# Kernel optimization log

Hardware: AMD Instinct MI355X
Metric: run time of the kernel (lower is better)

The kernel has to match this reference:

```python
import jax, jax.numpy as jnp
import numpy as np

B, L, D, H = 2, 2048, 512, 8
HS = D // H          # head_size = 64
BLOCK = 2048         # block_size
EPS = 1e-5


def setup_inputs() -> dict:
    key = jax.random.key(0)
    ks = jax.random.split(key, 8)
    s = 0.02
    x = jax.random.normal(ks[0], (B, L, D), jnp.float32)
    mask = jnp.triu(jnp.ones((1, 1, L, L), bool), k=1)  # causal: True above diag
    wq = jax.random.normal(ks[1], (D, D), jnp.float32) * s
    wk = jax.random.normal(ks[2], (D, D), jnp.float32) * s
    wv = jax.random.normal(ks[3], (D, D), jnp.float32) * s
    wo = jax.random.normal(ks[4], (D, D), jnp.float32) * s
    Er = jax.random.normal(ks[5], (H, BLOCK, HS), jnp.float32)
    bq = jnp.zeros((D,), jnp.float32)
    bk = jnp.zeros((D,), jnp.float32)
    bv = jnp.zeros((D,), jnp.float32)
    bo = jnp.zeros((D,), jnp.float32)
    ln_g = jnp.ones((D,), jnp.float32)
    ln_b = jnp.zeros((D,), jnp.float32)
    return dict(x=x, mask=mask, ln_g=ln_g, ln_b=ln_b, wq=wq, bq=bq,
                wk=wk, bk=bk, wv=wv, bv=bv, wo=wo, bo=bo, Er=Er)


def _skew(qe):
    # qe: [B, H, L, L] -> pad last dim on the left, reshape trick, drop first row
    padded = jnp.pad(qe, ((0, 0), (0, 0), (0, 0), (1, 0)))
    b, h, l, l1 = padded.shape
    return padded.reshape(b, h, l1, l)[:, :, 1:, :]


def reference(x, mask, ln_g, ln_b, wq, bq, wk, bk, wv, bv, wo, bo, Er):
    l = x.shape[1]
    # LayerNorm
    mu = jnp.mean(x, axis=-1, keepdims=True)
    var = jnp.mean((x - mu) ** 2, axis=-1, keepdims=True)
    hn = (x - mu) / jnp.sqrt(var + EPS) * ln_g + ln_b
    # QKV: [B, H, L, HS]
    q = (hn @ wq.T + bq).reshape(-1, l, H, HS).transpose(0, 2, 1, 3)
    k = (hn @ wk.T + bk).reshape(-1, l, H, HS).transpose(0, 2, 1, 3)
    v = (hn @ wv.T + bv).reshape(-1, l, H, HS).transpose(0, 2, 1, 3)
    # relative position bias via skew
    Ers = Er[:, BLOCK - l:, :]                       # [H, l, HS]
    QEr = jnp.einsum('bhld,hmd->bhlm', q, Ers)       # [B, H, L, L]
    SRel = _skew(QEr)
    # scaled dot-product scores
    w = jnp.einsum('bhld,bhmd->bhlm', q, k) * (HS ** -0.5)
    w = jnp.where(mask, -jnp.inf, w)
    SRel = jnp.where(mask, -jnp.inf, SRel)
    w = jax.nn.softmax(w + SRel, axis=-1)            # dropout omitted (eval mode)
    out = jnp.einsum('bhlm,bhmd->bhld', w, v)
    out = out.transpose(0, 2, 1, 3).reshape(-1, l, D)
    return out @ wo.T + bo
```

## Files before the change

kernel.cpp:

```cpp
#include <hip/hip_runtime.h>

#define LSEQ 2048
#define DIM 512
#define NH 8
#define HS 64

typedef __attribute__((ext_vector_type(8))) short short8;
typedef __attribute__((ext_vector_type(4))) float f32x4;

__device__ inline unsigned short f2bf(float f) {
  union { float f; unsigned u; } a; a.f = f;
  unsigned r = a.u + 0x7FFFu + ((a.u >> 16) & 1u);
  return (unsigned short)(r >> 16);
}
__device__ inline float bf2f(unsigned short h) {
  union { unsigned u; float f; } a; a.u = ((unsigned)h) << 16;
  return a.f;
}
__device__ inline unsigned cvtpk(float lo, float hi) {
  unsigned r;
  asm("v_cvt_pk_bf16_f32 %0, %1, %2" : "=v"(r) : "v"(lo), "v"(hi));
  return r;
}

__device__ inline f32x4 mfma_bf16(short8 a, short8 b, f32x4 c) {
  return __builtin_amdgcn_mfma_f32_16x16x32_bf16(a, b, c, 0, 0, 0);
}

__device__ inline short8 ld8(const unsigned short* p) {
  return *reinterpret_cast<const short8*>(p);
}

#define GLLDS(SRC, DST) __builtin_amdgcn_global_load_lds( \
    (const __attribute__((address_space(1))) void*)(SRC), \
    (__attribute__((address_space(3))) void*)(DST), 16, 0, 0)

__global__ __launch_bounds__(256) void cvt_all_kernel(
    const float* __restrict__ wq, const float* __restrict__ wk,
    const float* __restrict__ wv, const float* __restrict__ wo,
    const float* __restrict__ Er,
    unsigned short* __restrict__ wqb, unsigned short* __restrict__ wkb,
    unsigned short* __restrict__ wvb, unsigned short* __restrict__ wob,
    unsigned short* __restrict__ erb) {
  int b = blockIdx.x;
  const float* src; unsigned short* dst; int off;
  float scl = 1.f;
  if (b < 256)       { src = wq; dst = wqb; off = b; }
  else if (b < 512)  { src = wk; dst = wkb; off = b - 256; }
  else if (b < 768)  { src = wv; dst = wvb; off = b - 512; }
  else if (b < 1024) { src = wo; dst = wob; off = b - 768; }
  else               { src = Er; dst = erb; off = b - 1024; scl = 1.4426950408889634f; }
  int i = (off * 256 + threadIdx.x) * 4;
  float4 v = *reinterpret_cast<const float4*>(src + i);
  unsigned lo = (unsigned)f2bf(v.x * scl) | ((unsigned)f2bf(v.y * scl) << 16);
  unsigned hi = (unsigned)f2bf(v.z * scl) | ((unsigned)f2bf(v.w * scl) << 16);
  uint2 pk; pk.x = lo; pk.y = hi;
  *reinterpret_cast<uint2*>(dst + i) = pk;
}

__global__ __launch_bounds__(256) void ln_kernel(const float* __restrict__ x,
    const float* __restrict__ g, const float* __restrict__ bta,
    unsigned short* __restrict__ hn) {
  int lane = threadIdx.x & 63, w = threadIdx.x >> 6;
  int row = blockIdx.x * 4 + w;
  const float4* xr = reinterpret_cast<const float4*>(x + (size_t)row * DIM);
  float4 a = xr[2 * lane], c = xr[2 * lane + 1];
  float s = a.x + a.y + a.z + a.w + c.x + c.y + c.z + c.w;
  float sq = a.x * a.x + a.y * a.y + a.z * a.z + a.w * a.w +
             c.x * c.x + c.y * c.y + c.z * c.z + c.w * c.w;
#pragma unroll
  for (int off = 1; off < 64; off <<= 1) {
    s += __shfl_xor(s, off);
    sq += __shfl_xor(sq, off);
  }
  float mu = s * (1.f / DIM);
  float var = sq * (1.f / DIM) - mu * mu;
  float rstd = rsqrtf(var + 1e-5f);
  float4 g0 = reinterpret_cast<const float4*>(g)[2 * lane];
  float4 g1 = reinterpret_cast<const float4*>(g)[2 * lane + 1];
  float4 b0 = reinterpret_cast<const float4*>(bta)[2 * lane];
  float4 b1 = reinterpret_cast<const float4*>(bta)[2 * lane + 1];
  uint4 o;
  o.x = (unsigned)f2bf((a.x - mu) * rstd * g0.x + b0.x) |
        ((unsigned)f2bf((a.y - mu) * rstd * g0.y + b0.y) << 16);
  o.y = (unsigned)f2bf((a.z - mu) * rstd * g0.z + b0.z) |
        ((unsigned)f2bf((a.w - mu) * rstd * g0.w + b0.w) << 16);
  o.z = (unsigned)f2bf((c.x - mu) * rstd * g1.x + b1.x) |
        ((unsigned)f2bf((c.y - mu) * rstd * g1.y + b1.y) << 16);
  o.w = (unsigned)f2bf((c.z - mu) * rstd * g1.z + b1.z) |
        ((unsigned)f2bf((c.w - mu) * rstd * g1.w + b1.w) << 16);
  reinterpret_cast<uint4*>(hn)[(size_t)row * 64 + lane] = o;
}

__global__ __launch_bounds__(256, 3) void qkv_kernel(const unsigned short* __restrict__ hn,
    const unsigned short* __restrict__ wqb, const unsigned short* __restrict__ wkb,
    const unsigned short* __restrict__ wvb,
    const float* __restrict__ bq, const float* __restrict__ bk, const float* __restrict__ bv,
    unsigned short* __restrict__ qo, unsigned short* __restrict__ ko,
    unsigned short* __restrict__ vT) {
  __shared__ unsigned short As[3][128 * 32];
  __shared__ unsigned short Bs[3][128 * 32];
  int tid = threadIdx.x, lane = tid & 63, w = tid >> 6;
  int mcol = lane & 15, grp = lane >> 4;
  int l4 = lane >> 2, lql = lane & 3;
  int bid = blockIdx.x;
  int mat = bid >> 7;
  int rem = bid & 127;
  int m0 = (rem >> 2) << 7;
  int n0 = (rem & 3) << 7;
  const unsigned short* W = (mat == 0) ? wqb : (mat == 1) ? wkb : wvb;
  const float* bias = (mat == 0) ? bq : (mat == 1) ? bk : bv;
  float scl = (mat == 1) ? 0.18033688011112042f : 1.f;
  int wr = w >> 1, wc = w & 1;

  f32x4 acc[4][4];
#pragma unroll
  for (int i = 0; i < 4; ++i)
#pragma unroll
    for (int j = 0; j < 4; ++j) acc[i][j] = (f32x4){0.f, 0.f, 0.f, 0.f};

#pragma unroll
  for (int j = 0; j < 2; ++j) {
    int row = 32 * w + 16 * j + l4;
    GLLDS(hn + (size_t)(m0 + row) * DIM + lql * 8, &As[0][(32 * w + 16 * j) * 32]);
    GLLDS(W + (size_t)(n0 + row) * DIM + lql * 8, &Bs[0][(32 * w + 16 * j) * 32]);
  }
  for (int kk = 0; kk < 16; ++kk) {
    int buf = kk % 3;
    if (kk < 15) {
      int nbuf = (kk + 1) % 3;
      int k0 = (kk + 1) * 32;
#pragma unroll
      for (int j = 0; j < 2; ++j) {
        int row = 32 * w + 16 * j + l4;
        GLLDS(hn + (size_t)(m0 + row) * DIM + k0 + lql * 8, &As[nbuf][(32 * w + 16 * j) * 32]);
        GLLDS(W + (size_t)(n0 + row) * DIM + k0 + lql * 8, &Bs[nbuf][(32 * w + 16 * j) * 32]);
      }
      asm volatile("s_waitcnt vmcnt(4)\n\ts_barrier" ::: "memory");
    } else {
      asm volatile("s_waitcnt vmcnt(0)\n\ts_barrier" ::: "memory");
    }
    const unsigned short* AL = As[buf];
    const unsigned short* BL = Bs[buf];
    short8 af[4], bf[4];
#pragma unroll
    for (int f = 0; f < 4; ++f) {
      af[f] = ld8(&AL[(wr * 64 + f * 16 + mcol) * 32 + grp * 8]);
      bf[f] = ld8(&BL[(wc * 64 + f * 16 + mcol) * 32 + grp * 8]);
    }
#pragma unroll
    for (int fi = 0; fi < 4; ++fi)
#pragma unroll
      for (int fj = 0; fj < 4; ++fj)
        acc[fi][fj] = mfma_bf16(af[fi], bf[fj], acc[fi][fj]);
  }
#pragma unroll
  for (int fj = 0; fj < 4; ++fj) {
    int n = n0 + wc * 64 + fj * 16 + mcol;
    int hh = n >> 6, d = n & 63;
    float bsv = bias[n];
#pragma unroll
    for (int fi = 0; fi < 4; ++fi) {
#pragma unroll
      for (int r = 0; r < 4; ++r) {
        int m = m0 + wr * 64 + fi * 16 + 4 * grp + r;
        float val = (acc[fi][fj][r] + bsv) * scl;
        int b = m >> 11, l = m & (LSEQ - 1);
        unsigned short hv = f2bf(val);
        if (mat == 2) {
          size_t base = (size_t)(b * NH + hh) * HS * LSEQ;
          int idx = (((l >> 5) * 4 + (d >> 4)) * 64 + ((l >> 3) & 3) * 16 + (d & 15)) * 8 + (l & 7);
          vT[base + idx] = hv;
        } else {
          unsigned short* dst = (mat == 0) ? qo : ko;
          dst[((size_t)(b * NH + hh) * LSEQ + l) * HS + d] = hv;
        }
      }
    }
  }
}

__global__ __launch_bounds__(256, 2) void attn_kernel(const unsigned short* __restrict__ q,
    const unsigned short* __restrict__ k, const unsigned short* __restrict__ vT,
    const unsigned short* __restrict__ erb, char* __restrict__ partials) {
  __shared__ unsigned short Kt[2][64 * 64];
  __shared__ unsigned short Ers[320 * 64];
  __shared__ float Uall[4][16 * 84];
  int tid = threadIdx.x, lane = tid & 63, w = tid >> 6;
  int mcol = lane & 15, grp = lane >> 4;
  float* U = Uall[w];

  int bid = blockIdx.x;
  int xcd = bid & 7, s = bid >> 3;
  int hi2 = (s >= 80) ? 1 : 0;
  int bh = xcd + 8 * hi2;
  int ub = 79 - (s - 80 * hi2);
  int gp = (ub < 8) ? 0 : (ub < 24) ? 1 : (ub < 48) ? 2 : 3;
  int st0 = (gp == 0) ? 0 : (gp == 1) ? 8 : (gp == 2) ? 24 : 48;
  int idx = ub - st0;
  int tq = idx / (gp + 1);
  int cc = idx - tq * (gp + 1);
  int t64 = 8 * gp + tq;
  int qi0 = t64 << 6;
  int c0 = cc << 9;
  int kend = min(c0 + 512, qi0 + 64);
  int nkb = (kend - c0 + 63) >> 6;
  int h = bh & 7;

  const unsigned short* Qb = q + (size_t)bh * LSEQ * HS;
  const unsigned short* Kb = k + (size_t)bh * LSEQ * HS;
  const unsigned short* Vb = vT + (size_t)bh * HS * LSEQ;
  const unsigned short* Eb = erb + (size_t)h * LSEQ * HS;

  int qi0w = qi0 + 16 * w;
  short8 qf0 = ld8(Qb + (size_t)(qi0w + mcol) * HS + 8 * grp);
  short8 qf1 = ld8(Qb + (size_t)(qi0w + mcol) * HS + 32 + 8 * grp);
  int Estart = 2032 - qi0 - 48 + c0;
  int l8 = lane >> 3, lg = lane & 7;

#pragma unroll
  for (int j = 0; j < 2; ++j) {
    int row = 16 * w + 8 * j + l8;
    const unsigned short* src = Kb + (size_t)(c0 + row) * HS + (lg ^ (row & 7)) * 8;
    GLLDS(src, &Kt[0][(16 * w + 8 * j) * 64]);
  }
#pragma unroll
  for (int j = 0; j < 6; ++j) {
    int relb = 48 * w + 8 * j;
    int er = Estart + relb + l8;
    int erc = min(er, 2047);
    const unsigned short* src = Eb + (size_t)erc * HS + (lg ^ (er & 7)) * 8;
    GLLDS(src, &Ers[relb * 64]);
  }

  f32x4 o[4];
#pragma unroll
  for (int i = 0; i < 4; ++i) o[i] = (f32x4){0.f, 0.f, 0.f, 0.f};
  float lacc = 0.f;
  int srcA = mcol | ((grp & 1) << 5);
  int srcB = srcA + 16;
  bool hi = (grp >= 2);
  int efsw = mcol & 7;
  int ksw = mcol & 7;
  int vfoff = (grp * 16 + mcol) * 8;

  for (int kb = 0; kb < nkb; ++kb) {
    int kj0 = c0 + (kb << 6);
#pragma unroll
    for (int j = 0; j < 2; ++j) {
      int row = 16 * w + 8 * j + l8;
      int grow = min(kj0 + 64 + row, 2047);
      const unsigned short* src = Kb + (size_t)grow * HS + (lg ^ (row & 7)) * 8;
      GLLDS(src, &Kt[(kb + 1) & 1][(16 * w + 8 * j) * 64]);
    }
#pragma unroll
    for (int j = 0; j < 2; ++j) {
      int relb = 192 + 64 * kb + 16 * w + 8 * j;
      int ring = relb;
      if (ring >= 640) ring -= 640; else if (ring >= 320) ring -= 320;
      int er = Estart + relb + l8;
      int erc = min(er, 2047);
      const unsigned short* src = Eb + (size_t)erc * HS + (lg ^ (er & 7)) * 8;
      GLLDS(src, &Ers[ring * 64]);
    }
    asm volatile("s_waitcnt vmcnt(4)\n\ts_barrier" ::: "memory");
    short8 vf[8];
#pragma unroll
    for (int s2 = 0; s2 < 2; ++s2)
#pragma unroll
      for (int dt = 0; dt < 4; ++dt)
        vf[s2 * 4 + dt] = ld8(Vb + (size_t)(((kj0 >> 5) + s2) * 4 + dt) * 512 + vfoff);
#pragma unroll
    for (int jt = 0; jt < 5; ++jt) {
      int base16 = 48 - 16 * w + 64 * kb + 16 * jt;
      if (base16 >= 320) base16 -= 320;
      int slot = base16 + mcol;
      short8 ef0 = ld8(&Ers[slot * 64 + (grp ^ efsw) * 8]);
      short8 ef1 = ld8(&Ers[slot * 64 + ((4 + grp) ^ efsw) * 8]);
      f32x4 uu = (f32x4){0.f, 0.f, 0.f, 0.f};
      uu = mfma_bf16(ef0, qf0, uu);
      uu = mfma_bf16(ef1, qf1, uu);
      *reinterpret_cast<f32x4*>(&U[mcol * 84 + 16 * jt + 4 * grp]) = uu;
    }
    const unsigned short* KL = Kt[kb & 1];
    f32x4 stv[4];
#pragma unroll
    for (int t = 0; t < 4; ++t) {
      int row = 16 * t + mcol;
      short8 kf0 = ld8(&KL[row * 64 + (grp ^ ksw) * 8]);
      short8 kf1 = ld8(&KL[row * 64 + ((4 + grp) ^ ksw) * 8]);
      f32x4 a_ = (f32x4){0.f, 0.f, 0.f, 0.f};
      a_ = mfma_bf16(kf0, qf0, a_);
      a_ = mfma_bf16(kf1, qf1, a_);
      stv[t] = a_;
    }
    float lt[4][4];
    bool anymask = (kj0 + 63) > qi0w;
    if (anymask) {
#pragma unroll
      for (int t = 0; t < 4; ++t) {
        const float* up = &U[mcol * 84 + 16 * t + 4 * grp - mcol + 15];
#pragma unroll
        for (int r = 0; r < 4; ++r) {
          int n = 16 * t + 4 * grp + r;
          float val = stv[t][r] + up[r];
          val = (kj0 + n > qi0w + mcol) ? -1e30f : val;
          float p_ = exp2f(val);
          lt[t][r] = p_;
          lacc += p_;
        }
      }
    } else {
#pragma unroll
      for (int t = 0; t < 4; ++t) {
        const float* up = &U[mcol * 84 + 16 * t + 4 * grp - mcol + 15];
#pragma unroll
        for (int r = 0; r < 4; ++r) {
          float p_ = exp2f(stv[t][r] + up[r]);
          lt[t][r] = p_;
          lacc += p_;
        }
      }
    }
    unsigned w0[4], w1[4];
#pragma unroll
    for (int t = 0; t < 4; ++t) {
      w0[t] = cvtpk(lt[t][0], lt[t][1]);
      w1[t] = cvtpk(lt[t][2], lt[t][3]);
    }
#pragma unroll
    for (int s2 = 0; s2 < 2; ++s2) {
      unsigned y0a = (unsigned)__shfl((int)w0[2 * s2], srcA);
      unsigned y0b = (unsigned)__shfl((int)w0[2 * s2 + 1], srcA);
      unsigned y1a = (unsigned)__shfl((int)w1[2 * s2], srcA);
      unsigned y1b = (unsigned)__shfl((int)w1[2 * s2 + 1], srcA);
      unsigned y2a = (unsigned)__shfl((int)w0[2 * s2], srcB);
      unsigned y2b = (unsigned)__shfl((int)w0[2 * s2 + 1], srcB);
      unsigned y3a = (unsigned)__shfl((int)w1[2 * s2], srcB);
      unsigned y3b = (unsigned)__shfl((int)w1[2 * s2 + 1], srcB);
      union { unsigned u4[4]; short8 s8; } pu;
      pu.u4[0] = hi ? y0b : y0a;
      pu.u4[1] = hi ? y1b : y1a;
      pu.u4[2] = hi ? y2b : y2a;
      pu.u4[3] = hi ? y3b : y3a;
#pragma unroll
      for (int dt = 0; dt < 4; ++dt)
        o[dt] = mfma_bf16(vf[s2 * 4 + dt], pu.s8, o[dt]);
    }
  }

  float lsum = lacc;
  lsum += __shfl_xor(lsum, 16);
  lsum += __shfl_xor(lsum, 32);

  int pid = bh * 320 + ub * 4 + w;
  char* pb = partials + (size_t)pid * 2176;
  unsigned* Ob = (unsigned*)pb;
#pragma unroll
  for (int dt = 0; dt < 4; ++dt) {
    Ob[mcol * 32 + dt * 8 + grp * 2]     = cvtpk(o[dt][0], o[dt][1]);
    Ob[mcol * 32 + dt * 8 + grp * 2 + 1] = cvtpk(o[dt][2], o[dt][3]);
  }
  if (grp == 0) {
    ((float*)(pb + 2112))[mcol] = lsum;
  }
}

__global__ __launch_bounds__(256) void merge_kernel(const char* __restrict__ partials,
    unsigned short* __restrict__ attT) {
  int lane = threadIdx.x & 63, widx = threadIdx.x >> 6;
  int bid = blockIdx.x;
  int xcd = bid & 7, q_ = bid >> 3;
  int hi2 = (q_ >= 32) ? 1 : 0;
  int bh = xcd + 8 * hi2;
  int i = (q_ - 32 * hi2) * 4 + widx;
  int t64 = i >> 2, w = i & 3;
  int gp = t64 >> 3, tq = t64 & 7;
  int st0 = (gp == 0) ? 0 : (gp == 1) ? 8 : (gp == 2) ? 24 : 48;
  int nch = gp + 1;
  int row = lane >> 2, d0 = (lane & 3) << 4;
  float acc[16];
#pragma unroll
  for (int j = 0; j < 16; ++j) acc[j] = 0.f;
  float lsum = 0.f;
  for (int c = 0; c < nch; ++c) {
    int pid = bh * 320 + (st0 + tq * nch + c) * 4 + w;
    const char* pb = partials + (size_t)pid * 2176;
    lsum += ((const float*)(pb + 2112))[row];
    short8 v0 = *reinterpret_cast<const short8*>(pb + row * 128 + d0 * 2);
    short8 v1 = *reinterpret_cast<const short8*>(pb + row * 128 + d0 * 2 + 16);
#pragma unroll
    for (int j = 0; j < 8; ++j) {
      acc[j]     += bf2f((unsigned short)v0[j]);
      acc[8 + j] += bf2f((unsigned short)v1[j]);
    }
  }
  float inv = 1.f / lsum;
  int b = bh >> 3, h = bh & 7;
  unsigned short* dst = attT + ((size_t)(b * LSEQ) + i * 16 + row) * DIM + h * HS + d0;
  union { unsigned short us[16]; short8 s8[2]; } ou;
#pragma unroll
  for (int j = 0; j < 16; ++j) ou.us[j] = f2bf(acc[j] * inv);
  *reinterpret_cast<short8*>(dst) = ou.s8[0];
  *reinterpret_cast<short8*>(dst + 8) = ou.s8[1];
}

__global__ __launch_bounds__(256, 3) void out_kernel(const unsigned short* __restrict__ attT,
    const unsigned short* __restrict__ wob, const float* __restrict__ bo,
    float* __restrict__ out) {
  __shared__ unsigned short As[3][128 * 32];
  __shared__ unsigned short Bs[3][64 * 32];
  int tid = threadIdx.x, lane = tid & 63, w = tid >> 6;
  int mcol = lane & 15, grp = lane >> 4;
  int l4 = lane >> 2, lql = lane & 3;
  int bid = blockIdx.x;
  int m0 = (bid >> 3) << 7;
  int n0 = (bid & 7) << 6;
  int wr = w >> 1, wc = w & 1;

  f32x4 acc[4][2];
#pragma unroll
  for (int i = 0; i < 4; ++i)
#pragma unroll
    for (int j = 0; j < 2; ++j) acc[i][j] = (f32x4){0.f, 0.f, 0.f, 0.f};

#pragma unroll
  for (int j = 0; j < 2; ++j) {
    int row = 32 * w + 16 * j + l4;
    GLLDS(attT + (size_t)(m0 + row) * DIM + lql * 8, &As[0][(32 * w + 16 * j) * 32]);
  }
  {
    int row = 16 * w + l4;
    GLLDS(wob + (size_t)(n0 + row) * DIM + lql * 8, &Bs[0][(16 * w) * 32]);
  }
  for (int kk = 0; kk < 16; ++kk) {
    int buf = kk % 3;
    if (kk < 15) {
      int nbuf = (kk + 1) % 3;
      int k0 = (kk + 1) * 32;
#pragma unroll
      for (int j = 0; j < 2; ++j) {
        int row = 32 * w + 16 * j + l4;
        GLLDS(attT + (size_t)(m0 + row) * DIM + k0 + lql * 8, &As[nbuf][(32 * w + 16 * j) * 32]);
      }
      {
        int row = 16 * w + l4;
        GLLDS(wob + (size_t)(n0 + row) * DIM + k0 + lql * 8, &Bs[nbuf][(16 * w) * 32]);
      }
      asm volatile("s_waitcnt vmcnt(3)\n\ts_barrier" ::: "memory");
    } else {
      asm volatile("s_waitcnt vmcnt(0)\n\ts_barrier" ::: "memory");
    }
    const unsigned short* AL = As[buf];
    const unsigned short* BL = Bs[buf];
    short8 af[4], bf[2];
#pragma unroll
    for (int f = 0; f < 4; ++f)
      af[f] = ld8(&AL[(wr * 64 + f * 16 + mcol) * 32 + grp * 8]);
#pragma unroll
    for (int f = 0; f < 2; ++f)
      bf[f] = ld8(&BL[(wc * 32 + f * 16 + mcol) * 32 + grp * 8]);
#pragma unroll
    for (int fi = 0; fi < 4; ++fi)
#pragma unroll
      for (int fj = 0; fj < 2; ++fj)
        acc[fi][fj] = mfma_bf16(af[fi], bf[fj], acc[fi][fj]);
  }
#pragma unroll
  for (int fj = 0; fj < 2; ++fj) {
    int n = n0 + wc * 32 + fj * 16 + mcol;
    float bsv = bo[n];
#pragma unroll
    for (int fi = 0; fi < 4; ++fi) {
#pragma unroll
      for (int r = 0; r < 4; ++r) {
        int m = m0 + wr * 64 + fi * 16 + 4 * grp + r;
        out[(size_t)m * DIM + n] = acc[fi][fj][r] + bsv;
      }
    }
  }
}

extern "C" void kernel_launch(void* const* d_in, const int* in_sizes, int n_in,
                              void* d_out, int out_size, void* d_ws, size_t ws_size,
                              hipStream_t stream) {
  const float* x    = (const float*)d_in[0];
  const float* ln_g = (const float*)d_in[2];
  const float* ln_b = (const float*)d_in[3];
  const float* wq   = (const float*)d_in[4];
  const float* bq   = (const float*)d_in[5];
  const float* wk   = (const float*)d_in[6];
  const float* bk   = (const float*)d_in[7];
  const float* wv   = (const float*)d_in[8];
  const float* bv   = (const float*)d_in[9];
  const float* wo   = (const float*)d_in[10];
  const float* bo   = (const float*)d_in[11];
  const float* Er   = (const float*)d_in[12];
  float* out = (float*)d_out;

  char* ws = (char*)d_ws;
  unsigned short* hn   = (unsigned short*)(ws);
  unsigned short* qb   = (unsigned short*)(ws + (4u << 20));
  unsigned short* kb   = (unsigned short*)(ws + (8u << 20));
  unsigned short* vT   = (unsigned short*)(ws + (12u << 20));
  unsigned short* erb  = (unsigned short*)(ws + (16u << 20));
  unsigned short* attT = (unsigned short*)(ws + (18u << 20));
  unsigned short* wqb  = (unsigned short*)(ws + (22u << 20));
  unsigned short* wkb  = wqb + 512 * 512;
  unsigned short* wvb  = wkb + 512 * 512;
  unsigned short* wob  = wvb + 512 * 512;
  char* partials       = ws + (24u << 20);

  cvt_all_kernel<<<2048, 256, 0, stream>>>(wq, wk, wv, wo, Er, wqb, wkb, wvb, wob, erb);
  ln_kernel<<<1024, 256, 0, stream>>>(x, ln_g, ln_b, hn);
  qkv_kernel<<<384, 256, 0, stream>>>(hn, wqb, wkb, wvb, bq, bk, bv, qb, kb, vT);
  attn_kernel<<<1280, 256, 0, stream>>>(qb, kb, vT, erb, partials);
  merge_kernel<<<512, 256, 0, stream>>>(partials, attT);
  out_kernel<<<256, 256, 0, stream>>>(attT, wob, bo, out);
}
```

Before: 89.33 us.

## Store K and Er in MFMA fragment layout and load directly from global

K and the relative-position table Er are now written in a fragment-major layout, so each lane's 16-byte MFMA operand is contiguous. The attention kernel drops its LDS staging of K and Er, including the double-buffered global_load_lds prefetch and the per-iteration barrier, and loads operands straight from global memory into registers. With less LDS per block, launch bounds are raised to allow 3 blocks per SM, trading explicit prefetch overlap for occupancy. Er tiles no longer overlap between waves, so reuse now depends on cache hits rather than the shared ring buffer.

```diff
diff --git a/kernel.cpp b/kernel.cpp
--- a/kernel.cpp
+++ b/kernel.cpp
@@ -34,6 +34,10 @@
 #define GLLDS(SRC, DST) __builtin_amdgcn_global_load_lds( \
     (const __attribute__((address_space(1))) void*)(SRC), \
     (__attribute__((address_space(3))) void*)(DST), 16, 0, 0)
+
+__device__ inline int frag_idx(int row, int d) {
+  return (((row >> 4) * 2 + (d >> 5)) << 9) + (((row & 15) + ((d >> 3) & 3) * 16) << 3) + (d & 7);
+}
 
 __global__ __launch_bounds__(256) void cvt_all_kernel(
     const float* __restrict__ wq, const float* __restrict__ wk,
@@ -43,19 +47,31 @@
     unsigned short* __restrict__ wvb, unsigned short* __restrict__ wob,
     unsigned short* __restrict__ erb) {
   int b = blockIdx.x;
-  const float* src; unsigned short* dst; int off;
-  float scl = 1.f;
-  if (b < 256)       { src = wq; dst = wqb; off = b; }
-  else if (b < 512)  { src = wk; dst = wkb; off = b - 256; }
-  else if (b < 768)  { src = wv; dst = wvb; off = b - 512; }
-  else if (b < 1024) { src = wo; dst = wob; off = b - 768; }
-  else               { src = Er; dst = erb; off = b - 1024; scl = 1.4426950408889634f; }
-  int i = (off * 256 + threadIdx.x) * 4;
-  float4 v = *reinterpret_cast<const float4*>(src + i);
-  unsigned lo = (unsigned)f2bf(v.x * scl) | ((unsigned)f2bf(v.y * scl) << 16);
-  unsigned hi = (unsigned)f2bf(v.z * scl) | ((unsigned)f2bf(v.w * scl) << 16);
-  uint2 pk; pk.x = lo; pk.y = hi;
-  *reinterpret_cast<uint2*>(dst + i) = pk;
+  if (b < 1024) {
+    const float* src; unsigned short* dst; int off;
+    if (b < 256)       { src = wq; dst = wqb; off = b; }
+    else if (b < 512)  { src = wk; dst = wkb; off = b - 256; }
+    else if (b < 768)  { src = wv; dst = wvb; off = b - 512; }
+    else               { src = wo; dst = wob; off = b - 768; }
+    int i = (off * 256 + threadIdx.x) * 4;
+    float4 v = *reinterpret_cast<const float4*>(src + i);
+    unsigned lo = (unsigned)f2bf(v.x) | ((unsigned)f2bf(v.y) << 16);
+    unsigned hi = (unsigned)f2bf(v.z) | ((unsigned)f2bf(v.w) << 16);
+    uint2 pk; pk.x = lo; pk.y = hi;
+    *reinterpret_cast<uint2*>(dst + i) = pk;
+  } else {
+    const float scl = 1.4426950408889634f;
+    int i = ((b - 1024) * 256 + threadIdx.x) * 4;
+    int hh = i >> 17;
+    int rem = i & ((1 << 17) - 1);
+    int er = rem >> 6, d = rem & 63;
+    float4 v = *reinterpret_cast<const float4*>(Er + i);
+    unsigned lo = (unsigned)f2bf(v.x * scl) | ((unsigned)f2bf(v.y * scl) << 16);
+    unsigned hi = (unsigned)f2bf(v.z * scl) | ((unsigned)f2bf(v.w * scl) << 16);
+    uint2 pk; pk.x = lo; pk.y = hi;
+    unsigned short* dst = erb + (size_t)hh * LSEQ * HS + frag_idx(er, d);
+    *reinterpret_cast<uint2*>(dst) = pk;
+  }
 }
 
 __global__ __launch_bounds__(256) void ln_kernel(const float* __restrict__ x,
@@ -167,24 +183,23 @@
         float val = (acc[fi][fj][r] + bsv) * scl;
         int b = m >> 11, l = m & (LSEQ - 1);
         unsigned short hv = f2bf(val);
+        size_t base = (size_t)(b * NH + hh) * HS * LSEQ;
         if (mat == 2) {
-          size_t base = (size_t)(b * NH + hh) * HS * LSEQ;
           int idx = (((l >> 5) * 4 + (d >> 4)) * 64 + ((l >> 3) & 3) * 16 + (d & 15)) * 8 + (l & 7);
           vT[base + idx] = hv;
+        } else if (mat == 1) {
+          ko[base + frag_idx(l, d)] = hv;
         } else {
-          unsigned short* dst = (mat == 0) ? qo : ko;
-          dst[((size_t)(b * NH + hh) * LSEQ + l) * HS + d] = hv;
+          qo[((size_t)(b * NH + hh) * LSEQ + l) * HS + d] = hv;
         }
       }
     }
   }
 }
 
-__global__ __launch_bounds__(256, 2) void attn_kernel(const unsigned short* __restrict__ q,
+__global__ __launch_bounds__(256, 3) void attn_kernel(const unsigned short* __restrict__ q,
     const unsigned short* __restrict__ k, const unsigned short* __restrict__ vT,
     const unsigned short* __restrict__ erb, char* __restrict__ partials) {
-  __shared__ unsigned short Kt[2][64 * 64];
-  __shared__ unsigned short Ers[320 * 64];
   __shared__ float Uall[4][16 * 84];
   int tid = threadIdx.x, lane = tid & 63, w = tid >> 6;
   int mcol = lane & 15, grp = lane >> 4;
@@ -215,23 +230,6 @@
   int qi0w = qi0 + 16 * w;
   short8 qf0 = ld8(Qb + (size_t)(qi0w + mcol) * HS + 8 * grp);
   short8 qf1 = ld8(Qb + (size_t)(qi0w + mcol) * HS + 32 + 8 * grp);
-  int Estart = 2032 - qi0 - 48 + c0;
-  int l8 = lane >> 3, lg = lane & 7;
-
-#pragma unroll
-  for (int j = 0; j < 2; ++j) {
-    int row = 16 * w + 8 * j + l8;
-    const unsigned short* src = Kb + (size_t)(c0 + row) * HS + (lg ^ (row & 7)) * 8;
-    GLLDS(src, &Kt[0][(16 * w + 8 * j) * 64]);
-  }
-#pragma unroll
-  for (int j = 0; j < 6; ++j) {
-    int relb = 48 * w + 8 * j;
-    int er = Estart + relb + l8;
-    int erc = min(er, 2047);
-    const unsigned short* src = Eb + (size_t)erc * HS + (lg ^ (er & 7)) * 8;
-    GLLDS(src, &Ers[relb * 64]);
-  }
 
   f32x4 o[4];
 #pragma unroll
@@ -240,58 +238,41 @@
   int srcA = mcol | ((grp & 1) << 5);
   int srcB = srcA + 16;
   bool hi = (grp >= 2);
-  int efsw = mcol & 7;
-  int ksw = mcol & 7;
-  int vfoff = (grp * 16 + mcol) * 8;
+  int loff = lane * 8;
 
   for (int kb = 0; kb < nkb; ++kb) {
     int kj0 = c0 + (kb << 6);
-#pragma unroll
-    for (int j = 0; j < 2; ++j) {
-      int row = 16 * w + 8 * j + l8;
-      int grow = min(kj0 + 64 + row, 2047);
-      const unsigned short* src = Kb + (size_t)grow * HS + (lg ^ (row & 7)) * 8;
-      GLLDS(src, &Kt[(kb + 1) & 1][(16 * w + 8 * j) * 64]);
-    }
-#pragma unroll
-    for (int j = 0; j < 2; ++j) {
-      int relb = 192 + 64 * kb + 16 * w + 8 * j;
-      int ring = relb;
-      if (ring >= 640) ring -= 640; else if (ring >= 320) ring -= 320;
-      int er = Estart + relb + l8;
-      int erc = min(er, 2047);
-      const unsigned short* src = Eb + (size_t)erc * HS + (lg ^ (er & 7)) * 8;
-      GLLDS(src, &Ers[ring * 64]);
-    }
-    asm volatile("s_waitcnt vmcnt(4)\n\ts_barrier" ::: "memory");
+    int E0w = 2032 - qi0w + kj0;
+    short8 kf[8];
+#pragma unroll
+    for (int t = 0; t < 4; ++t) {
+      int blk = ((kj0 >> 4) + t) * 2;
+      kf[2 * t]     = ld8(Kb + (size_t)blk * 512 + loff);
+      kf[2 * t + 1] = ld8(Kb + (size_t)(blk + 1) * 512 + loff);
+    }
     short8 vf[8];
 #pragma unroll
     for (int s2 = 0; s2 < 2; ++s2)
 #pragma unroll
       for (int dt = 0; dt < 4; ++dt)
-        vf[s2 * 4 + dt] = ld8(Vb + (size_t)(((kj0 >> 5) + s2) * 4 + dt) * 512 + vfoff);
+        vf[s2 * 4 + dt] = ld8(Vb + (size_t)(((kj0 >> 5) + s2) * 4 + dt) * 512 + loff);
 #pragma unroll
     for (int jt = 0; jt < 5; ++jt) {
-      int base16 = 48 - 16 * w + 64 * kb + 16 * jt;
-      if (base16 >= 320) base16 -= 320;
-      int slot = base16 + mcol;
-      short8 ef0 = ld8(&Ers[slot * 64 + (grp ^ efsw) * 8]);
-      short8 ef1 = ld8(&Ers[slot * 64 + ((4 + grp) ^ efsw) * 8]);
+      int g = (E0w >> 4) + jt;
+      if (g > 127) g = 127;
+      short8 ef0 = ld8(Eb + (size_t)(g * 2) * 512 + loff);
+      short8 ef1 = ld8(Eb + (size_t)(g * 2 + 1) * 512 + loff);
       f32x4 uu = (f32x4){0.f, 0.f, 0.f, 0.f};
       uu = mfma_bf16(ef0, qf0, uu);
       uu = mfma_bf16(ef1, qf1, uu);
       *reinterpret_cast<f32x4*>(&U[mcol * 84 + 16 * jt + 4 * grp]) = uu;
     }
-    const unsigned short* KL = Kt[kb & 1];
     f32x4 stv[4];
 #pragma unroll
     for (int t = 0; t < 4; ++t) {
-      int row = 16 * t + mcol;
-      short8 kf0 = ld8(&KL[row * 64 + (grp ^ ksw) * 8]);
-      short8 kf1 = ld8(&KL[row * 64 + ((4 + grp) ^ ksw) * 8]);
       f32x4 a_ = (f32x4){0.f, 0.f, 0.f, 0.f};
-      a_ = mfma_bf16(kf0, qf0, a_);
-      a_ = mfma_bf16(kf1, qf1, a_);
+      a_ = mfma_bf16(kf[2 * t], qf0, a_);
+      a_ = mfma_bf16(kf[2 * t + 1], qf1, a_);
       stv[t] = a_;
     }
     float lt[4][4];
```

New measurement: 83.45 us. 1.07x faster.
